# Kernel tuning notes

Hardware: AMD Instinct MI355X
Metric: run time of the kernel (lower is better)

## Reference

```python
import jax, jax.numpy as jnp
import numpy as np

B, S, D = 2, 512, 1024   # batch, seq, hidden_size
E, K, I = 16, 8, 1024    # num_experts, num_experts_per_tok, moe_intermediate_size
I_SH = 1024              # moe_intermediate_size * num_shared_experts
ROUTE_SCALE = 2.826


def setup_inputs() -> dict:
    key = jax.random.key(0)
    ks = jax.random.split(key, 8)
    s = 0.02
    return {
        "x": jax.random.normal(ks[0], (B, S, D), dtype=jnp.float32),
        "gate_w": jax.random.normal(ks[1], (E, D), dtype=jnp.float32) * s,
        "expert_bias": jnp.zeros((E,), dtype=jnp.float32),
        "w_gate": jax.random.normal(ks[2], (E, I, D), dtype=jnp.float32) * s,
        "w_up": jax.random.normal(ks[3], (E, I, D), dtype=jnp.float32) * s,
        "w_down": jax.random.normal(ks[4], (E, D, I), dtype=jnp.float32) * s,
        "shared_gate_w": jax.random.normal(ks[5], (I_SH, D), dtype=jnp.float32) * s,
        "shared_up_w": jax.random.normal(ks[6], (I_SH, D), dtype=jnp.float32) * s,
        "shared_down_w": jax.random.normal(ks[7], (D, I_SH), dtype=jnp.float32) * s,
    }


def reference(x, gate_w, expert_bias, w_gate, w_up, w_down,
              shared_gate_w, shared_up_w, shared_down_w):
    # --- routing (sigmoid scores, top-k, optional norm, scale) ---
    gates = jnp.einsum('bsd,ed->bse', x, gate_w)
    scores = jax.nn.sigmoid(gates.astype(jnp.float32))           # [B,S,E]
    sel_scores = scores + expert_bias
    _, inds = jax.lax.top_k(sel_scores, K)                       # [B,S,K]
    selected = jnp.take_along_axis(scores, inds, axis=-1)        # [B,S,K]
    selected = selected / selected.sum(axis=-1, keepdims=True)   # route_norm (K>1)
    selected = selected * ROUTE_SCALE
    # combine weights as dense [B,S,E]; unselected experts get weight 0,
    # which is mathematically identical to gather-dispatch-combine.
    onehot = jax.nn.one_hot(inds, E, dtype=selected.dtype)       # [B,S,K,E]
    combine = jnp.einsum('bske,bsk->bse', onehot, selected)
    # --- experts (SwitchGLU: per-expert SwiGLU MLPs) ---
    hg = jnp.einsum('bsd,eid->bsei', x, w_gate)                  # [B,S,E,I]
    hu = jnp.einsum('bsd,eid->bsei', x, w_up)
    h = jax.nn.silu(hg) * hu
    ye = jnp.einsum('bsei,edi->bsed', h, w_down)                 # [B,S,E,D]
    y = jnp.einsum('bsed,bse->bsd', ye, combine).astype(x.dtype)
    # --- shared expert MLP (SwiGLU) ---
    g = jnp.einsum('bsd,id->bsi', x, shared_gate_w)
    u = jnp.einsum('bsd,id->bsi', x, shared_up_w)
    y = y + jnp.einsum('bsi,di->bsd', jax.nn.silu(g) * u, shared_down_w)
    return y
```

## Files before the change

kernel.cpp:

```cpp
#include <hip/hip_runtime.h>
#include <hip/hip_bf16.h>


typedef __attribute__((ext_vector_type(8))) short bf16x8;
typedef __attribute__((ext_vector_type(4))) float f32x4;

#define NTOK 1024
#define DD   1024
#define II   1024
#define NE   16
#define NEXP 17
#define KSEL 8
#define RSCALE 2.826f

#define BM 128
#define BN 64
#define BK 32
#define LDA 40

#define MB (1024ull*1024ull)
#define OFF_XBF   0ull
#define OFF_H     (2ull*MB)
#define OFF_WG    (36ull*MB)
#define OFF_WU    (70ull*MB)
#define OFF_WD    (104ull*MB)
#define OFF_LIST  (138ull*MB)
#define OFF_SCALE (OFF_LIST + 4ull*NEXP*NTOK)
#define OFF_CNT   (OFF_SCALE + 4ull*NEXP*NTOK)
#define WS_NEED   (OFF_CNT + 4096ull)

__device__ __forceinline__ unsigned short f2bf(float f) {
    union { __hip_bfloat16 h; unsigned short u; } c;
    c.h = __float2bfloat16(f);
    return c.u;
}

__device__ __forceinline__ void gl2lds16(const unsigned short* g, unsigned short* l) {
    __builtin_amdgcn_global_load_lds(
        (const __attribute__((address_space(1))) void*)g,
        (__attribute__((address_space(3))) void*)l, 16, 0, 0);
}

__global__ __launch_bounds__(256) void prep_kernel(
    const float* __restrict__ x, unsigned short* __restrict__ xbf,
    int* __restrict__ list, float* __restrict__ scalebuf, int* __restrict__ count)
{
    int idx = blockIdx.x * 256 + threadIdx.x;
    float4 v = ((const float4*)x)[idx];
    ((ushort4*)xbf)[idx] = make_ushort4(f2bf(v.x), f2bf(v.y), f2bf(v.z), f2bf(v.w));
    if (idx < NTOK) { list[NE * NTOK + idx] = idx; scalebuf[NE * NTOK + idx] = 1.0f; }
    if (idx == 0) count[NE] = NTOK;
}

__global__ __launch_bounds__(256) void wconv_kernel(
    const float* __restrict__ wg, const float* __restrict__ wu, const float* __restrict__ wd,
    const float* __restrict__ sgw, const float* __restrict__ suw, const float* __restrict__ sdw,
    unsigned short* __restrict__ wgb, unsigned short* __restrict__ wub,
    unsigned short* __restrict__ wdb)
{
    size_t i4 = (size_t)blockIdx.x * 256 + threadIdx.x;
    const size_t ROUTED4 = (size_t)NE * II * DD / 4;
    int p = blockIdx.y;
    const float* rsrc = (p == 0) ? wg : (p == 1) ? wu : wd;
    const float* ssrc = (p == 0) ? sgw : (p == 1) ? suw : sdw;
    unsigned short* dst = (p == 0) ? wgb : (p == 1) ? wub : wdb;
    const float* src = (i4 < ROUTED4) ? rsrc + 4 * i4 : ssrc + 4 * (i4 - ROUTED4);
    float4 v = *(const float4*)src;
    ((ushort4*)dst)[i4] = make_ushort4(f2bf(v.x), f2bf(v.y), f2bf(v.z), f2bf(v.w));
}

__global__ __launch_bounds__(256) void route_score_kernel(
    const float* __restrict__ x, const float* __restrict__ gw,
    const float* __restrict__ bias,
    unsigned int* __restrict__ emask, float* __restrict__ tsc)
{
    int wave = threadIdx.x >> 6, lane = threadIdx.x & 63;
    int t = blockIdx.x * 4 + wave;

    const float4* xr = (const float4*)(x + (size_t)t * DD);
    float acc[NE];
#pragma unroll
    for (int e = 0; e < NE; e++) acc[e] = 0.f;
#pragma unroll
    for (int i = 0; i < DD / 64 / 4; i++) {
        float4 xv = xr[lane + 64 * i];
#pragma unroll
        for (int e = 0; e < NE; e++) {
            float4 w = ((const float4*)(gw + (size_t)e * DD))[lane + 64 * i];
            acc[e] += xv.x * w.x + xv.y * w.y + xv.z * w.z + xv.w * w.w;
        }
    }
#pragma unroll
    for (int e = 0; e < NE; e++) {
        float v = acc[e];
        for (int off = 32; off > 0; off >>= 1) v += __shfl_xor(v, off, 64);
        acc[e] = v;
    }
    if (lane == 0) {
        float sc[NE], sel[NE];
#pragma unroll
        for (int e = 0; e < NE; e++) {
            sc[e] = 1.f / (1.f + expf(-acc[e]));
            sel[e] = sc[e] + bias[e];
        }
        bool used[NE] = {};
        int inds[KSEL];
        float ssum = 0.f;
        for (int k = 0; k < KSEL; k++) {
            float best = -1e30f; int bi = 0;
            for (int e = 0; e < NE; e++)
                if (!used[e] && sel[e] > best) { best = sel[e]; bi = e; }
            used[bi] = true; inds[k] = bi; ssum += sc[bi];
        }
        float inv = RSCALE / ssum;
        unsigned int m = 0;
        for (int k = 0; k < KSEL; k++) {
            int e = inds[k];
            m |= (1u << e);
            tsc[(size_t)t * NE + e] = sc[e] * inv;
        }
        emask[t] = m;
    }
}

__global__ __launch_bounds__(1024) void build_lists_kernel(
    const unsigned int* __restrict__ emask, const float* __restrict__ tsc,
    int* __restrict__ count, int* __restrict__ list, float* __restrict__ scalebuf)
{
    int e = blockIdx.x;
    int t = threadIdx.x;
    int lane = t & 63, wave = t >> 6;
    bool sel = (emask[t] >> e) & 1u;
    unsigned long long m = __ballot(sel);
    int posw = __popcll(m & ((1ull << lane) - 1ull));
    int wtot = __popcll(m);
    __shared__ int woff[16];
    if (lane == 0) woff[wave] = wtot;
    __syncthreads();
    if (t == 0) {
        int s = 0;
#pragma unroll
        for (int w = 0; w < 16; w++) { int v = woff[w]; woff[w] = s; s += v; }
        count[e] = s;
    }
    __syncthreads();
    if (sel) {
        int pos = woff[wave] + posw;
        list[e * NTOK + pos] = t;
        scalebuf[e * NTOK + pos] = tsc[(size_t)t * NE + e];
    }
}

__global__ __launch_bounds__(256, 2) void gateup_kernel(
    const unsigned short* __restrict__ xbf,
    const unsigned short* __restrict__ wgb, const unsigned short* __restrict__ wub,
    const int* __restrict__ count, const int* __restrict__ list,
    const float* __restrict__ scalebuf, unsigned short* __restrict__ hbuf)
{
    int s = blockIdx.x;
    int xcd = s & 7, t = s >> 3;
    int g = xcd + 8 * (t >> 3);
    int e = g >> 3;
    int n0 = (g & 7) * 128;
    int m0 = (t & 7) * 128;
    int cnt = count[e];
    if (m0 >= cnt) return;
    const unsigned short* Bg = wgb + (size_t)e * II * DD;
    const unsigned short* Bu = wub + (size_t)e * II * DD;

    __shared__ __align__(16) unsigned short As[8192];
    __shared__ __align__(16) unsigned short Bgs[8192];
    __shared__ __align__(16) unsigned short Bus[8192];
    __shared__ int rowtok[128];

    int tid = threadIdx.x;
    if (tid < 128) {
        int gr = m0 + tid;
        rowtok[tid] = list[e * NTOK + ((gr < cnt) ? gr : (cnt - 1))];
    }
    __syncthreads();

    int lane = tid & 63, wave = tid >> 6;
    int wm = wave & 1, wn = wave >> 1;
    int row16 = lane & 15, quad = lane >> 4;

    int qS = wave >> 1;
    int srow = (wave & 1) * 64 + (lane >> 2);
    int colS = ((lane & 3) ^ ((lane >> 3) & 3)) * 8;
    int tokr[4];
#pragma unroll
    for (int c = 0; c < 4; c++) tokr[c] = rowtok[srow + c * 16];
    const unsigned short* gBg0 = Bg + (size_t)(n0 + srow) * DD + colS;
    const unsigned short* gBu0 = Bu + (size_t)(n0 + srow) * DD + colS;

    f32x4 accG[4][4], accU[4][4];
#pragma unroll
    for (int mi = 0; mi < 4; mi++)
#pragma unroll
        for (int ni = 0; ni < 4; ni++) {
            accG[mi][ni] = (f32x4){0.f, 0.f, 0.f, 0.f};
            accU[mi][ni] = (f32x4){0.f, 0.f, 0.f, 0.f};
        }

    int qe = (quad ^ ((row16 >> 1) & 3)) * 8;

    for (int k0 = 0; k0 < DD; k0 += 64) {
        int koff = k0 + qS * 32;
#pragma unroll
        for (int c = 0; c < 4; c++) {
            gl2lds16(xbf + (size_t)tokr[c] * DD + koff + colS, As + wave * 2048 + c * 512);
            gl2lds16(gBg0 + (size_t)(c * 16) * DD + koff, Bgs + wave * 2048 + c * 512);
            gl2lds16(gBu0 + (size_t)(c * 16) * DD + koff, Bus + wave * 2048 + c * 512);
        }
        __syncthreads();

#pragma unroll
        for (int kk = 0; kk < 2; kk++) {
            bf16x8 a[4], bg[4], bu[4];
            int base = kk * 4096 + qe;
#pragma unroll
            for (int mi = 0; mi < 4; mi++)
                a[mi] = *(const bf16x8*)(As + base + (wm * 64 + mi * 16 + row16) * 32);
#pragma unroll
            for (int ni = 0; ni < 4; ni++) {
                bg[ni] = *(const bf16x8*)(Bgs + base + (wn * 64 + ni * 16 + row16) * 32);
                bu[ni] = *(const bf16x8*)(Bus + base + (wn * 64 + ni * 16 + row16) * 32);
            }
#pragma unroll
            for (int mi = 0; mi < 4; mi++)
#pragma unroll
                for (int ni = 0; ni < 4; ni++) {
                    accG[mi][ni] = __builtin_amdgcn_mfma_f32_16x16x32_bf16(a[mi], bg[ni], accG[mi][ni], 0, 0, 0);
                    accU[mi][ni] = __builtin_amdgcn_mfma_f32_16x16x32_bf16(a[mi], bu[ni], accU[mi][ni], 0, 0, 0);
                }
        }
        __syncthreads();
    }

#pragma unroll
    for (int mi = 0; mi < 4; mi++) {
        int grb = m0 + wm * 64 + mi * 16 + quad * 4;
#pragma unroll
        for (int r = 0; r < 4; r++) {
            int gr = grb + r;
            if (gr >= cnt) continue;
            float rs = scalebuf[e * NTOK + gr];
            size_t rowoff = ((size_t)e * NTOK + gr) * II + n0 + wn * 64;
#pragma unroll
            for (int ni = 0; ni < 4; ni++) {
                float g2 = accG[mi][ni][r], u = accU[mi][ni][r];
                float h = g2 / (1.f + __expf(-g2)) * u * rs;
                hbuf[rowoff + ni * 16 + row16] = f2bf(h);
            }
        }
    }
}

__global__ __launch_bounds__(256, 3) void down_kernel(
    const unsigned short* __restrict__ hbuf,
    const unsigned short* __restrict__ wdb,
    const int* __restrict__ count, const int* __restrict__ list,
    float* __restrict__ y)
{
    int s = blockIdx.x;
    int xcd = s & 7, t = s >> 3;
    int g = xcd + 8 * (t >> 3);
    int e = g >> 3;
    int n0 = (g & 7) * 128;
    int m0 = (t & 7) * 128;
    int cnt = count[e];
    if (m0 >= cnt) return;
    const unsigned short* Bp = wdb + (size_t)e * DD * II;

    __shared__ __align__(16) unsigned short As[8192];
    __shared__ __align__(16) unsigned short Bs[8192];

    int tid = threadIdx.x;
    int lane = tid & 63, wave = tid >> 6;
    int wm = wave & 1, wn = wave >> 1;
    int row16 = lane & 15, quad = lane >> 4;

    int qS = wave >> 1;
    int srow = (wave & 1) * 64 + (lane >> 2);
    int colS = ((lane & 3) ^ ((lane >> 3) & 3)) * 8;

    size_t arow[4];
#pragma unroll
    for (int c = 0; c < 4; c++) {
        int gr = m0 + srow + c * 16;
        int idx = (gr < cnt) ? gr : (cnt - 1);
        arow[c] = ((size_t)e * NTOK + idx) * II;
    }
    const unsigned short* gB0 = Bp + (size_t)(n0 + srow) * II + colS;

    f32x4 acc[4][4];
#pragma unroll
    for (int mi = 0; mi < 4; mi++)
#pragma unroll
        for (int ni = 0; ni < 4; ni++) acc[mi][ni] = (f32x4){0.f, 0.f, 0.f, 0.f};

    int qe = (quad ^ ((row16 >> 1) & 3)) * 8;

    for (int k0 = 0; k0 < II; k0 += 64) {
        int koff = k0 + qS * 32;
#pragma unroll
        for (int c = 0; c < 4; c++) {
            gl2lds16(hbuf + arow[c] + koff + colS, As + wave * 2048 + c * 512);
            gl2lds16(gB0 + (size_t)(c * 16) * II + koff, Bs + wave * 2048 + c * 512);
        }
        __syncthreads();

#pragma unroll
        for (int kk = 0; kk < 2; kk++) {
            bf16x8 a[4], b[4];
            int base = kk * 4096 + qe;
#pragma unroll
            for (int mi = 0; mi < 4; mi++)
                a[mi] = *(const bf16x8*)(As + base + (wm * 64 + mi * 16 + row16) * 32);
#pragma unroll
            for (int ni = 0; ni < 4; ni++)
                b[ni] = *(const bf16x8*)(Bs + base + (wn * 64 + ni * 16 + row16) * 32);
#pragma unroll
            for (int mi = 0; mi < 4; mi++)
#pragma unroll
                for (int ni = 0; ni < 4; ni++)
                    acc[mi][ni] = __builtin_amdgcn_mfma_f32_16x16x32_bf16(a[mi], b[ni], acc[mi][ni], 0, 0, 0);
        }
        __syncthreads();
    }

#pragma unroll
    for (int mi = 0; mi < 4; mi++) {
        int grb = m0 + wm * 64 + mi * 16 + quad * 4;
#pragma unroll
        for (int r = 0; r < 4; r++) {
            int gr = grb + r;
            if (gr >= cnt) continue;
            int tk = list[e * NTOK + gr];
            float* yr = y + (size_t)tk * DD + n0 + wn * 64;
#pragma unroll
            for (int ni = 0; ni < 4; ni++)
                unsafeAtomicAdd(yr + ni * 16 + row16, acc[mi][ni][r]);
        }
    }
}

__global__ __launch_bounds__(256) void gateup_fb(
    const unsigned short* __restrict__ xbf,
    const float* __restrict__ wg, const float* __restrict__ wu,
    const float* __restrict__ sgw, const float* __restrict__ suw,
    const int* __restrict__ count, const int* __restrict__ list,
    const float* __restrict__ scalebuf, unsigned short* __restrict__ hbuf)
{
    int e = blockIdx.z;
    int cnt = count[e];
    int m0 = blockIdx.x * BM;
    if (m0 >= cnt) return;
    int n0 = blockIdx.y * BN;
    const float* Bg = (e < NE) ? wg + (size_t)e * II * DD : sgw;
    const float* Bu = (e < NE) ? wu + (size_t)e * II * DD : suw;

    __shared__ __align__(16) unsigned short As[BM * LDA];
    __shared__ __align__(16) unsigned short Bgs[BN * LDA];
    __shared__ __align__(16) unsigned short Bus[BN * LDA];
    __shared__ int rowtok[BM];

    int tid = threadIdx.x;
    if (tid < BM) {
        int gr = m0 + tid;
        rowtok[tid] = (gr < cnt) ? list[e * NTOK + gr] : -1;
    }
    __syncthreads();

    int lane = tid & 63, wave = tid >> 6;
    int wm = wave >> 1, wn = wave & 1;
    int row16 = lane & 15, quad = lane >> 4;

    f32x4 accG[4][2], accU[4][2];
#pragma unroll
    for (int mi = 0; mi < 4; mi++)
#pragma unroll
        for (int ni = 0; ni < 2; ni++) {
            accG[mi][ni] = (f32x4){0.f, 0.f, 0.f, 0.f};
            accU[mi][ni] = (f32x4){0.f, 0.f, 0.f, 0.f};
        }

    for (int k0 = 0; k0 < DD; k0 += BK) {
#pragma unroll
        for (int i = 0; i < 2; i++) {
            int c = tid + 256 * i;
            int row = c >> 2, kc = (c & 3) * 8;
            int tok = rowtok[row];
            uint4 v = (tok >= 0) ? *(const uint4*)(xbf + (size_t)tok * DD + k0 + kc)
                                 : make_uint4(0u, 0u, 0u, 0u);
            *(uint4*)(As + row * LDA + kc) = v;
        }
#pragma unroll
        for (int i = 0; i < 2; i++) {
            int c = tid + 256 * i;
            int row = c >> 3, f = (c & 7) * 4;
            float4 vg = *(const float4*)(Bg + (size_t)(n0 + row) * DD + k0 + f);
            float4 vu = *(const float4*)(Bu + (size_t)(n0 + row) * DD + k0 + f);
            *(ushort4*)(Bgs + row * LDA + f) = make_ushort4(f2bf(vg.x), f2bf(vg.y), f2bf(vg.z), f2bf(vg.w));
            *(ushort4*)(Bus + row * LDA + f) = make_ushort4(f2bf(vu.x), f2bf(vu.y), f2bf(vu.z), f2bf(vu.w));
        }
        __syncthreads();

        bf16x8 af[4], bg[2], bu[2];
#pragma unroll
        for (int mi = 0; mi < 4; mi++)
            af[mi] = *(const bf16x8*)(As + (wm * 64 + mi * 16 + row16) * LDA + quad * 8);
#pragma unroll
        for (int ni = 0; ni < 2; ni++) {
            bg[ni] = *(const bf16x8*)(Bgs + (wn * 32 + ni * 16 + row16) * LDA + quad * 8);
            bu[ni] = *(const bf16x8*)(Bus + (wn * 32 + ni * 16 + row16) * LDA + quad * 8);
        }
#pragma unroll
        for (int mi = 0; mi < 4; mi++)
#pragma unroll
            for (int ni = 0; ni < 2; ni++) {
                accG[mi][ni] = __builtin_amdgcn_mfma_f32_16x16x32_bf16(af[mi], bg[ni], accG[mi][ni], 0, 0, 0);
                accU[mi][ni] = __builtin_amdgcn_mfma_f32_16x16x32_bf16(af[mi], bu[ni], accU[mi][ni], 0, 0, 0);
            }
        __syncthreads();
    }

#pragma unroll
    for (int mi = 0; mi < 4; mi++) {
        int mbase = wm * 64 + mi * 16 + quad * 4;
#pragma unroll
        for (int r = 0; r < 4; r++) {
            int gr = m0 + mbase + r;
            if (gr >= cnt) continue;
            float rs = scalebuf[e * NTOK + gr];
            size_t rowoff = ((size_t)e * NTOK + gr) * II + n0;
#pragma unroll
            for (int ni = 0; ni < 2; ni++) {
                int n = wn * 32 + ni * 16 + row16;
                float g = accG[mi][ni][r], u = accU[mi][ni][r];
                float h = g / (1.f + __expf(-g)) * u * rs;
                hbuf[rowoff + n] = f2bf(h);
            }
        }
    }
}

__global__ __launch_bounds__(256) void down_fb(
    const unsigned short* __restrict__ hbuf,
    const float* __restrict__ wd, const float* __restrict__ sdw,
    const int* __restrict__ count, const int* __restrict__ list,
    float* __restrict__ y)
{
    int e = blockIdx.z;
    int cnt = count[e];
    int m0 = blockIdx.x * BM;
    if (m0 >= cnt) return;
    int n0 = blockIdx.y * BN;
    const float* Bp = (e < NE) ? wd + (size_t)e * DD * II : sdw;

    __shared__ __align__(16) unsigned short As[BM * LDA];
    __shared__ __align__(16) unsigned short Bs[BN * LDA];

    int tid = threadIdx.x;
    int lane = tid & 63, wave = tid >> 6;
    int wm = wave >> 1, wn = wave & 1;
    int row16 = lane & 15, quad = lane >> 4;

    f32x4 acc[4][2];
#pragma unroll
    for (int mi = 0; mi < 4; mi++)
#pragma unroll
        for (int ni = 0; ni < 2; ni++) acc[mi][ni] = (f32x4){0.f, 0.f, 0.f, 0.f};

    const unsigned short* Abase = hbuf + ((size_t)e * NTOK + m0) * II;

    for (int k0 = 0; k0 < II; k0 += BK) {
#pragma unroll
        for (int i = 0; i < 2; i++) {
            int c = tid + 256 * i;
            int row = c >> 2, kc = (c & 3) * 8;
            uint4 v = (m0 + row < cnt) ? *(const uint4*)(Abase + (size_t)row * II + k0 + kc)
                                       : make_uint4(0u, 0u, 0u, 0u);
            *(uint4*)(As + row * LDA + kc) = v;
        }
#pragma unroll
        for (int i = 0; i < 2; i++) {
            int c = tid + 256 * i;
            int row = c >> 3, f = (c & 7) * 4;
            float4 v = *(const float4*)(Bp + (size_t)(n0 + row) * II + k0 + f);
            *(ushort4*)(Bs + row * LDA + f) = make_ushort4(f2bf(v.x), f2bf(v.y), f2bf(v.z), f2bf(v.w));
        }
        __syncthreads();

        bf16x8 af[4], bf[2];
#pragma unroll
        for (int mi = 0; mi < 4; mi++)
            af[mi] = *(const bf16x8*)(As + (wm * 64 + mi * 16 + row16) * LDA + quad * 8);
#pragma unroll
        for (int ni = 0; ni < 2; ni++)
            bf[ni] = *(const bf16x8*)(Bs + (wn * 32 + ni * 16 + row16) * LDA + quad * 8);
#pragma unroll
        for (int mi = 0; mi < 4; mi++)
#pragma unroll
            for (int ni = 0; ni < 2; ni++)
                acc[mi][ni] = __builtin_amdgcn_mfma_f32_16x16x32_bf16(af[mi], bf[ni], acc[mi][ni], 0, 0, 0);
        __syncthreads();
    }

#pragma unroll
    for (int mi = 0; mi < 4; mi++) {
        int mbase = wm * 64 + mi * 16 + quad * 4;
#pragma unroll
        for (int r = 0; r < 4; r++) {
            int gr = m0 + mbase + r;
            if (gr >= cnt) continue;
            int t = list[e * NTOK + gr];
#pragma unroll
            for (int ni = 0; ni < 2; ni++) {
                int n = wn * 32 + ni * 16 + row16;
                unsafeAtomicAdd(&y[(size_t)t * DD + n0 + n], acc[mi][ni][r]);
            }
        }
    }
}

extern "C" void kernel_launch(void* const* d_in, const int* in_sizes, int n_in,
                              void* d_out, int out_size, void* d_ws, size_t ws_size,
                              hipStream_t stream)
{
    const float* x    = (const float*)d_in[0];
    const float* gw   = (const float*)d_in[1];
    const float* bias = (const float*)d_in[2];
    const float* wg   = (const float*)d_in[3];
    const float* wu   = (const float*)d_in[4];
    const float* wd   = (const float*)d_in[5];
    const float* sgw  = (const float*)d_in[6];
    const float* suw  = (const float*)d_in[7];
    const float* sdw  = (const float*)d_in[8];
    float* y = (float*)d_out;

    char* ws = (char*)d_ws;
    unsigned short* xbf  = (unsigned short*)(ws + OFF_XBF);
    unsigned short* hbuf = (unsigned short*)(ws + OFF_H);
    unsigned short* wgb  = (unsigned short*)(ws + OFF_WG);
    unsigned short* wub  = (unsigned short*)(ws + OFF_WU);
    unsigned short* wdb  = (unsigned short*)(ws + OFF_WD);
    int*   list     = (int*)(ws + OFF_LIST);
    float* scalebuf = (float*)(ws + OFF_SCALE);
    int*   count    = (int*)(ws + OFF_CNT);

    bool big = (ws_size >= WS_NEED);
    if (!big) {
        list     = (int*)(ws + 36ull * MB);
        scalebuf = (float*)(ws + 36ull * MB + 4ull * NEXP * NTOK);
        count    = (int*)(ws + 36ull * MB + 8ull * NEXP * NTOK);
    }

    unsigned int* emask = (unsigned int*)(ws + OFF_H);
    float*        tsc   = (float*)(ws + OFF_H + 4096);

    hipMemsetAsync(d_out, 0, (size_t)NTOK * DD * sizeof(float), stream);

    prep_kernel<<<dim3(NTOK * DD / 4 / 256), 256, 0, stream>>>(x, xbf, list, scalebuf, count);
    route_score_kernel<<<dim3(NTOK / 4), 256, 0, stream>>>(x, gw, bias, emask, tsc);
    build_lists_kernel<<<dim3(NE), 1024, 0, stream>>>(emask, tsc, count, list, scalebuf);

    if (big) {
        wconv_kernel<<<dim3((unsigned)((size_t)NEXP * II * DD / 4 / 256), 3), 256, 0, stream>>>(
            wg, wu, wd, sgw, suw, sdw, wgb, wub, wdb);
        gateup_kernel<<<dim3(NEXP * 8 * 8), 256, 0, stream>>>(
            xbf, wgb, wub, count, list, scalebuf, hbuf);
        down_kernel<<<dim3(NEXP * 8 * 8), 256, 0, stream>>>(
            hbuf, wdb, count, list, y);
    } else {
        gateup_fb<<<dim3(NTOK / BM, II / BN, NEXP), 256, 0, stream>>>(
            xbf, wg, wu, sgw, suw, count, list, scalebuf, hbuf);
        down_fb<<<dim3(NTOK / BM, DD / BN, NEXP), 256, 0, stream>>>(
            hbuf, wd, sdw, count, list, y);
    }
}
```

Baseline: 396.1 us.

## Fuse prep, routing and weight conversion into one prologue kernel

Merges the x-to-bf16 conversion into the routing score kernel and runs the weight fp32-to-bf16 conversion as extra blocks of the same launch. Weight conversion now uses wider nontemporal loads with 8 elements per thread per chunk. The shared-expert list setup moves into an extra block of build_lists. The aim is fewer launches and better streaming bandwidth for the dominant weight conversion. It also adds an unused poslut output path, which is currently passed as null.

```diff
diff --git a/kernel.cpp b/kernel.cpp
--- a/kernel.cpp
+++ b/kernel.cpp
@@ -4,6 +4,7 @@
 
 typedef __attribute__((ext_vector_type(8))) short bf16x8;
 typedef __attribute__((ext_vector_type(4))) float f32x4;
+typedef __attribute__((ext_vector_type(8))) unsigned short u16x8;
 
 #define NTOK 1024
 #define DD   1024
@@ -12,6 +13,9 @@
 #define NEXP 17
 #define KSEL 8
 #define RSCALE 2.826f
+
+#define WCONV_BLOCKS 1088
+#define ROUTE_BLOCKS 256
 
 #define BM 128
 #define BN 64
@@ -41,49 +45,60 @@
         (__attribute__((address_space(3))) void*)l, 16, 0, 0);
 }
 
-__global__ __launch_bounds__(256) void prep_kernel(
-    const float* __restrict__ x, unsigned short* __restrict__ xbf,
-    int* __restrict__ list, float* __restrict__ scalebuf, int* __restrict__ count)
-{
-    int idx = blockIdx.x * 256 + threadIdx.x;
-    float4 v = ((const float4*)x)[idx];
-    ((ushort4*)xbf)[idx] = make_ushort4(f2bf(v.x), f2bf(v.y), f2bf(v.z), f2bf(v.w));
-    if (idx < NTOK) { list[NE * NTOK + idx] = idx; scalebuf[NE * NTOK + idx] = 1.0f; }
-    if (idx == 0) count[NE] = NTOK;
-}
-
-__global__ __launch_bounds__(256) void wconv_kernel(
+__device__ __forceinline__ f32x4 ntload4(const float* p) {
+    return __builtin_nontemporal_load((const f32x4*)p);
+}
+
+__global__ __launch_bounds__(256) void prologue_kernel(
+    const float* __restrict__ x, const float* __restrict__ gw,
+    const float* __restrict__ bias, unsigned short* __restrict__ xbf,
+    unsigned int* __restrict__ emask, float* __restrict__ tsc,
     const float* __restrict__ wg, const float* __restrict__ wu, const float* __restrict__ wd,
     const float* __restrict__ sgw, const float* __restrict__ suw, const float* __restrict__ sdw,
     unsigned short* __restrict__ wgb, unsigned short* __restrict__ wub,
     unsigned short* __restrict__ wdb)
 {
-    size_t i4 = (size_t)blockIdx.x * 256 + threadIdx.x;
-    const size_t ROUTED4 = (size_t)NE * II * DD / 4;
-    int p = blockIdx.y;
-    const float* rsrc = (p == 0) ? wg : (p == 1) ? wu : wd;
-    const float* ssrc = (p == 0) ? sgw : (p == 1) ? suw : sdw;
-    unsigned short* dst = (p == 0) ? wgb : (p == 1) ? wub : wdb;
-    const float* src = (i4 < ROUTED4) ? rsrc + 4 * i4 : ssrc + 4 * (i4 - ROUTED4);
-    float4 v = *(const float4*)src;
-    ((ushort4*)dst)[i4] = make_ushort4(f2bf(v.x), f2bf(v.y), f2bf(v.z), f2bf(v.w));
-}
-
-__global__ __launch_bounds__(256) void route_score_kernel(
-    const float* __restrict__ x, const float* __restrict__ gw,
-    const float* __restrict__ bias,
-    unsigned int* __restrict__ emask, float* __restrict__ tsc)
-{
+    if (blockIdx.x >= ROUTE_BLOCKS) {
+        int wb = blockIdx.x - ROUTE_BLOCKS;
+        int p  = wb / WCONV_BLOCKS;
+        int bx = wb - p * WCONV_BLOCKS;
+        const size_t ROUTED8 = (size_t)NE * II * DD / 8;
+        const float* rsrc = (p == 0) ? wg : (p == 1) ? wu : wd;
+        const float* ssrc = (p == 0) ? sgw : (p == 1) ? suw : sdw;
+        unsigned short* dst = (p == 0) ? wgb : (p == 1) ? wub : wdb;
+
+        size_t base8 = (size_t)bx * 2048 + threadIdx.x;
+        f32x4 a[8], b[8];
+#pragma unroll
+        for (int c = 0; c < 8; c++) {
+            size_t g8 = base8 + c * 256;
+            const float* src = (g8 < ROUTED8) ? rsrc + 8 * g8 : ssrc + 8 * (g8 - ROUTED8);
+            a[c] = ntload4(src);
+            b[c] = ntload4(src + 4);
+        }
+#pragma unroll
+        for (int c = 0; c < 8; c++) {
+            size_t g8 = base8 + c * 256;
+            u16x8 o;
+            o[0] = f2bf(a[c][0]); o[1] = f2bf(a[c][1]); o[2] = f2bf(a[c][2]); o[3] = f2bf(a[c][3]);
+            o[4] = f2bf(b[c][0]); o[5] = f2bf(b[c][1]); o[6] = f2bf(b[c][2]); o[7] = f2bf(b[c][3]);
+            *(u16x8*)(dst + 8 * g8) = o;
+        }
+        return;
+    }
+
     int wave = threadIdx.x >> 6, lane = threadIdx.x & 63;
     int t = blockIdx.x * 4 + wave;
 
     const float4* xr = (const float4*)(x + (size_t)t * DD);
+    ushort4* xw = (ushort4*)(xbf + (size_t)t * DD);
     float acc[NE];
 #pragma unroll
     for (int e = 0; e < NE; e++) acc[e] = 0.f;
 #pragma unroll
     for (int i = 0; i < DD / 64 / 4; i++) {
         float4 xv = xr[lane + 64 * i];
+        xw[lane + 64 * i] = make_ushort4(f2bf(xv.x), f2bf(xv.y), f2bf(xv.z), f2bf(xv.w));
 #pragma unroll
         for (int e = 0; e < NE; e++) {
             float4 w = ((const float4*)(gw + (size_t)e * DD))[lane + 64 * i];
@@ -125,10 +140,17 @@
 
 __global__ __launch_bounds__(1024) void build_lists_kernel(
     const unsigned int* __restrict__ emask, const float* __restrict__ tsc,
-    int* __restrict__ count, int* __restrict__ list, float* __restrict__ scalebuf)
+    int* __restrict__ count, int* __restrict__ list, float* __restrict__ scalebuf,
+    int* __restrict__ poslut)
 {
     int e = blockIdx.x;
     int t = threadIdx.x;
+    if (e == NE) {
+        list[NE * NTOK + t] = t;
+        scalebuf[NE * NTOK + t] = 1.0f;
+        if (t == 0) count[NE] = NTOK;
+        return;
+    }
     int lane = t & 63, wave = t >> 6;
     bool sel = (emask[t] >> e) & 1u;
     unsigned long long m = __ballot(sel);
@@ -144,11 +166,12 @@
         count[e] = s;
     }
     __syncthreads();
+    int pos = woff[wave] + posw;
     if (sel) {
-        int pos = woff[wave] + posw;
         list[e * NTOK + pos] = t;
         scalebuf[e * NTOK + pos] = tsc[(size_t)t * NE + e];
     }
+    if (poslut) poslut[e * NTOK + t] = sel ? pos : -1;
 }
 
 __global__ __launch_bounds__(256, 2) void gateup_kernel(
@@ -561,13 +584,14 @@
 
     hipMemsetAsync(d_out, 0, (size_t)NTOK * DD * sizeof(float), stream);
 
-    prep_kernel<<<dim3(NTOK * DD / 4 / 256), 256, 0, stream>>>(x, xbf, list, scalebuf, count);
-    route_score_kernel<<<dim3(NTOK / 4), 256, 0, stream>>>(x, gw, bias, emask, tsc);
-    build_lists_kernel<<<dim3(NE), 1024, 0, stream>>>(emask, tsc, count, list, scalebuf);
+    unsigned pro_grid = big ? (ROUTE_BLOCKS + 3 * WCONV_BLOCKS) : ROUTE_BLOCKS;
+    prologue_kernel<<<dim3(pro_grid), 256, 0, stream>>>(
+        x, gw, bias, xbf, emask, tsc,
+        wg, wu, wd, sgw, suw, sdw, wgb, wub, wdb);
+    build_lists_kernel<<<dim3(NEXP), 1024, 0, stream>>>(emask, tsc, count, list, scalebuf,
+                                                        (int*)nullptr);
 
     if (big) {
-        wconv_kernel<<<dim3((unsigned)((size_t)NEXP * II * DD / 4 / 256), 3), 256, 0, stream>>>(
-            wg, wu, wd, sgw, suw, sdw, wgb, wub, wdb);
         gateup_kernel<<<dim3(NEXP * 8 * 8), 256, 0, stream>>>(
             xbf, wgb, wub, count, list, scalebuf, hbuf);
         down_kernel<<<dim3(NEXP * 8 * 8), 256, 0, stream>>>(
```

Result: faster. 349.2 us (-11.9%).
